# Kernel optimization log

Hardware: AMD Instinct MI355X
Metric: run time of the kernel (lower is better)

## Reference

```python
import jax, jax.numpy as jnp
import numpy as np

B, N, L, D_MODEL, H, D_K, D_V = 8, 307, 64, 64, 4, 16, 16


def setup_inputs() -> dict:
    key = jax.random.key(0)
    ks = jax.random.split(key, 10)
    inp = {
        "input_Q": jax.random.normal(ks[0], (B, N, L, D_MODEL), jnp.float32),
        "input_K": jax.random.normal(ks[1], (B, N, L, D_MODEL), jnp.float32),
        "input_V": jax.random.normal(ks[2], (B, N, L, D_MODEL), jnp.float32),
        "attn_mask": jax.random.uniform(ks[3], (B, N, L, 1), jnp.float32),
        "res_att": jax.random.normal(ks[4], (B, N, H, L, L), jnp.float32),
        # Linear weights stored as [in, out] (torch nn.Linear weight transposed)
        "W_Q": jax.random.normal(ks[5], (D_MODEL, H * D_K), jnp.float32) / np.sqrt(D_MODEL),
        "W_K": jax.random.normal(ks[6], (D_MODEL, H * D_K), jnp.float32) / np.sqrt(D_MODEL),
        "W_V": jax.random.normal(ks[7], (D_MODEL, H * D_V), jnp.float32) / np.sqrt(D_MODEL),
        "W_fc": jax.random.normal(ks[8], (H * D_V, D_MODEL), jnp.float32) / np.sqrt(H * D_V),
        # freshly-constructed nn.LayerNorm has weight=1, bias=0
        "ln_scale": jnp.ones((D_MODEL,), jnp.float32),
        "ln_bias": jnp.zeros((D_MODEL,), jnp.float32),
    }
    return inp


def _layernorm(x, scale, bias, eps=1e-5):
    mu = jnp.mean(x, axis=-1, keepdims=True)
    var = jnp.mean(jnp.square(x - mu), axis=-1, keepdims=True)
    return (x - mu) * jax.lax.rsqrt(var + eps) * scale + bias


def reference(input_Q, input_K, input_V, attn_mask, res_att, W_Q, W_K, W_V, W_fc, ln_scale, ln_bias):
    # projections -> [B,N,H,L,d]
    def proj(x, W, d):
        y = jnp.einsum('bnlf,fe->bnle', x, W)
        return y.reshape(B, N, L, H, d).transpose(0, 1, 3, 2, 4)

    Q = proj(input_Q, W_Q, D_K)
    K = proj(input_K, W_K, D_K)
    V = proj(input_V, W_V, D_V)

    # scaled QK^T + residual attention bias: [B,N,H,Lq,Lk]
    scores = jnp.einsum('bnhqd,bnhkd->bnhqk', Q, K) / np.sqrt(D_K) + res_att
    # attn_mask [B,N,L,1] -> broadcast over heads (axis 2) and key dim (last)
    mask = attn_mask[:, :, None, :, :]  # [B,N,1,L,1]
    scores = jnp.where(mask > 0.5, jnp.float32(-1e9), scores)

    # NOTE: original softmaxes over dim=3 (the query axis), faithful here
    attn = jax.nn.softmax(scores, axis=3)
    context = jnp.einsum('bnhqk,bnhkd->bnhqd', attn, V)
    context = context.transpose(0, 1, 3, 2, 4).reshape(B, N, L, H * D_V)
    output = jnp.einsum('bnlc,cf->bnlf', context, W_fc)
    out = _layernorm(output + input_Q, ln_scale, ln_bias)
    return out, scores
```

## Files before the change

### kernel.cpp

```cpp
#include <hip/hip_runtime.h>

#define B_   8
#define N_   307
#define BN   (B_ * N_)
#define OUT_ELEMS (BN * 64 * 64)

typedef float f32x4 __attribute__((ext_vector_type(4)));
typedef short s16x8 __attribute__((ext_vector_type(8)));

__device__ __forceinline__ unsigned short f2bf(float x) {
    unsigned int u = __builtin_bit_cast(unsigned int, x);
    u += 0x7FFFu + ((u >> 16) & 1u);
    return (unsigned short)(u >> 16);
}

__device__ __forceinline__ void bar_lds() {
    asm volatile("s_waitcnt lgkmcnt(0)\n\ts_barrier" ::: "memory");
}

__device__ __forceinline__ int swz(int row) { return row ^ ((row >> 3) & 7); }

__device__ __forceinline__ s16x8 ldfrag(const unsigned short* p) {
    return *reinterpret_cast<const s16x8*>(p);
}

__device__ __forceinline__ s16x8 cvt8(float4 lo, float4 hi) {
    s16x8 f;
    f[0] = (short)f2bf(lo.x); f[1] = (short)f2bf(lo.y);
    f[2] = (short)f2bf(lo.z); f[3] = (short)f2bf(lo.w);
    f[4] = (short)f2bf(hi.x); f[5] = (short)f2bf(hi.y);
    f[6] = (short)f2bf(hi.z); f[7] = (short)f2bf(hi.w);
    return f;
}

__device__ __forceinline__ void loadW(const float* __restrict__ src,
                                      float4 wvv[4], int tid) {
    const float4* s4 = reinterpret_cast<const float4*>(src);
#pragma unroll
    for (int i = 0; i < 4; ++i) wvv[i] = s4[i * 256 + tid];
}

__device__ __forceinline__ void writeW(const float4 wvv[4],
                                       unsigned short* dst, int tid) {
#pragma unroll
    for (int i = 0; i < 4; ++i) {
        int idx = i * 256 + tid;
        float4 v = wvv[i];
        int k  = idx >> 4;
        int n0 = (idx & 15) << 2;
        int ki = k >> 5;
        int qd = (k >> 3) & 3;
        int j  = k & 7;
        float vv[4] = {v.x, v.y, v.z, v.w};
#pragma unroll
        for (int c = 0; c < 4; ++c) {
            int n = n0 + c;
            int row = ((n >> 4) * 2 + ki) * 64 + (qd << 4) + (n & 15);
            dst[(swz(row) << 3) + j] = f2bf(vv[c]);
        }
    }
}

__global__ __launch_bounds__(256, 4) void mta_kernel(
    const float* __restrict__ Xq, const float* __restrict__ Xk,
    const float* __restrict__ Xv, const float* __restrict__ maskp,
    const float* __restrict__ res, const float* __restrict__ Wq,
    const float* __restrict__ Wk, const float* __restrict__ Wv,
    const float* __restrict__ Wfc, const float* __restrict__ lnS,
    const float* __restrict__ lnB, float* __restrict__ out,
    float* __restrict__ scores_out)
{
    __shared__ __align__(16) unsigned char smem[40960];
    unsigned short* sKf = (unsigned short*)(smem);
    unsigned short* sQf = (unsigned short*)(smem + 8192);
    unsigned short* sVf = (unsigned short*)(smem + 16384);
    unsigned short* sW0 = (unsigned short*)(smem + 24576);
    unsigned short* sW1 = (unsigned short*)(smem + 32768);

    const int bn   = blockIdx.x;
    const int tid  = threadIdx.x;
    const int w    = tid >> 6;
    const int lane = tid & 63;
    const int quad = lane >> 4;
    const int l16  = lane & 15;
    const size_t base64 = (size_t)bn * 4096;

    const int soff0 = l16 * 64 + w * 16 + quad * 4;

    bool bmv[4];
#pragma unroll
    for (int nt = 0; nt < 4; ++nt)
        bmv[nt] = maskp[bn * 64 + nt * 16 + l16] > 0.5f;

    const int xoff = (w * 16 + l16) * 64 + quad * 8;
    float4 wv[4];
    loadW(Wq, wv, tid);
    const float* pX0 = Xq + base64 + xoff;
    float4 x00 = *(const float4*)(pX0),      x01 = *(const float4*)(pX0 + 4);
    float4 x02 = *(const float4*)(pX0 + 32), x03 = *(const float4*)(pX0 + 36);
    f32x4 rA[4];
    {
        const float* rp = res + (((size_t)(bn * 4)) << 12) + soff0;
#pragma unroll
        for (int nt = 0; nt < 4; ++nt)
            rA[nt] = *reinterpret_cast<const f32x4*>(rp + nt * 1024);
    }
    writeW(wv, sW0, tid);
    bar_lds();

    loadW(Wk, wv, tid);
    const float* pX1 = Xk + base64 + xoff;
    float4 x10 = *(const float4*)(pX1),      x11 = *(const float4*)(pX1 + 4);
    float4 x12 = *(const float4*)(pX1 + 32), x13 = *(const float4*)(pX1 + 36);
    {
        s16x8 a0 = cvt8(x00, x01);
        s16x8 a1 = cvt8(x02, x03);
#pragma unroll
        for (int nt = 0; nt < 4; ++nt) {
            f32x4 acc = {0.f, 0.f, 0.f, 0.f};
            s16x8 b0 = ldfrag(sW0 + (swz((nt * 2 + 0) * 64 + lane) << 3));
            s16x8 b1 = ldfrag(sW0 + (swz((nt * 2 + 1) * 64 + lane) << 3));
            acc = __builtin_amdgcn_mfma_f32_16x16x32_bf16(a0, b0, acc, 0, 0, 0);
            acc = __builtin_amdgcn_mfma_f32_16x16x32_bf16(a1, b1, acc, 0, 0, 0);
#pragma unroll
            for (int r = 0; r < 4; ++r) {
                int rowq = (nt * 4 + w) * 32 + ((l16 >> 3) << 4) + quad * 4 + r;
                sQf[(swz(rowq) << 3) + (l16 & 7)] = f2bf(acc[r] * 0.25f);
            }
        }
    }
    writeW(wv, sW1, tid);
    bar_lds();

    loadW(Wv, wv, tid);
    const float* pX2 = Xv + base64 + xoff;
    float4 x20 = *(const float4*)(pX2),      x21 = *(const float4*)(pX2 + 4);
    float4 x22 = *(const float4*)(pX2 + 32), x23 = *(const float4*)(pX2 + 36);
    {
        s16x8 a0 = cvt8(x10, x11);
        s16x8 a1 = cvt8(x12, x13);
#pragma unroll
        for (int nt = 0; nt < 4; ++nt) {
            f32x4 acc = {0.f, 0.f, 0.f, 0.f};
            s16x8 b0 = ldfrag(sW1 + (swz((nt * 2 + 0) * 64 + lane) << 3));
            s16x8 b1 = ldfrag(sW1 + (swz((nt * 2 + 1) * 64 + lane) << 3));
            acc = __builtin_amdgcn_mfma_f32_16x16x32_bf16(a0, b0, acc, 0, 0, 0);
            acc = __builtin_amdgcn_mfma_f32_16x16x32_bf16(a1, b1, acc, 0, 0, 0);
#pragma unroll
            for (int r = 0; r < 4; ++r) {
                int rowk = (nt * 4 + w) * 32 + ((l16 >> 3) << 4) + quad * 4 + r;
                sKf[(swz(rowk) << 3) + (l16 & 7)] = f2bf(acc[r]);
            }
        }
    }
    writeW(wv, sW0, tid);
    bar_lds();

    {
        s16x8 a0 = cvt8(x20, x21);
        s16x8 a1 = cvt8(x22, x23);
#pragma unroll
        for (int nt = 0; nt < 4; ++nt) {
            f32x4 acc = {0.f, 0.f, 0.f, 0.f};
            s16x8 b0 = ldfrag(sW0 + (swz((nt * 2 + 0) * 64 + lane) << 3));
            s16x8 b1 = ldfrag(sW0 + (swz((nt * 2 + 1) * 64 + lane) << 3));
            acc = __builtin_amdgcn_mfma_f32_16x16x32_bf16(a0, b0, acc, 0, 0, 0);
            acc = __builtin_amdgcn_mfma_f32_16x16x32_bf16(a1, b1, acc, 0, 0, 0);
#pragma unroll
            for (int r = 0; r < 4; ++r) {
                int kk = w * 16 + quad * 4 + r;
                int rowv = (nt * 2 + (kk >> 5)) * 64 + (((kk >> 3) & 3) << 4) + l16;
                sVf[(swz(rowv) << 3) + (kk & 7)] = f2bf(acc[r]);
            }
        }
    }
    bar_lds();

    f32x4 ctx[4];
#pragma unroll
    for (int h = 0; h < 4; ++h) ctx[h] = {0.f, 0.f, 0.f, 0.f};

    float4 wfc[4];
    float xres[4][4], scl[4], bia[4];
    const int toff = (w * 16 + quad * 4) * 64 + l16;

    const s16x8 zf = {0, 0, 0, 0, 0, 0, 0, 0};
#pragma unroll
    for (int h = 0; h < 4; ++h) {
        const size_t sbase = ((size_t)(bn * 4 + h)) << 12;
        unsigned short* buf = (h & 1) ? sW1 : sW0;

        s16x8 bk = zf;
        if (lane < 32) bk = ldfrag(sKf + (swz((h * 4 + w) * 32 + lane) << 3));

        f32x4 sr[4];
        float ev[4][4];
        float esum[4] = {0.f, 0.f, 0.f, 0.f};
#pragma unroll
        for (int nt = 0; nt < 4; ++nt) {
            s16x8 aq = zf;
            if (lane < 32) aq = ldfrag(sQf + (swz((h * 4 + nt) * 32 + lane) << 3));
            f32x4 t = __builtin_amdgcn_mfma_f32_16x16x32_bf16(bk, aq, rA[nt], 0, 0, 0);
#pragma unroll
            for (int r = 0; r < 4; ++r) {
                float s = bmv[nt] ? -1e9f : t[r];
                sr[nt][r] = s;
                float e = __expf(s);
                ev[nt][r] = e;
                esum[r] += e;
            }
        }
#pragma unroll
        for (int m = 1; m <= 8; m <<= 1)
#pragma unroll
            for (int r = 0; r < 4; ++r)
                esum[r] += __shfl_xor(esum[r], m, 64);
        float inv[4];
#pragma unroll
        for (int r = 0; r < 4; ++r) inv[r] = 1.0f / (esum[r] + 1e-30f);

#pragma unroll
        for (int nt = 0; nt < 4; ++nt) {
            int row = (nt * 2 + (w >> 1)) * 64 + (((w & 1) << 1) + (quad >> 1)) * 16 + l16;
            short4 pk;
            pk.x = (short)f2bf(ev[nt][0] * inv[0]);
            pk.y = (short)f2bf(ev[nt][1] * inv[1]);
            pk.z = (short)f2bf(ev[nt][2] * inv[2]);
            pk.w = (short)f2bf(ev[nt][3] * inv[3]);
            *reinterpret_cast<short4*>(buf + (swz(row) << 3) + ((quad & 1) << 2)) = pk;
        }
        bar_lds();

        if (h < 3) {
            const float* rp2 = res + sbase + 4096 + soff0;
#pragma unroll
            for (int nt = 0; nt < 4; ++nt)
                rA[nt] = *reinterpret_cast<const f32x4*>(rp2 + nt * 1024);
        } else {
            loadW(Wfc, wfc, tid);
            const float* xp = Xq + base64 + toff;
#pragma unroll
            for (int nt = 0; nt < 4; ++nt) {
#pragma unroll
                for (int r = 0; r < 4; ++r) xres[nt][r] = xp[r * 64 + nt * 16];
                scl[nt] = lnS[nt * 16 + l16];
                bia[nt] = lnB[nt * 16 + l16];
            }
        }
#pragma unroll
        for (int nt = 0; nt < 4; ++nt)
            *reinterpret_cast<f32x4*>(scores_out + sbase + soff0 + nt * 1024) = sr[nt];

#pragma unroll
        for (int ki = 0; ki < 2; ++ki) {
            s16x8 ap = ldfrag(buf + (swz((w * 2 + ki) * 64 + lane) << 3));
            s16x8 bv = ldfrag(sVf + (swz((h * 2 + ki) * 64 + lane) << 3));
            ctx[h] = __builtin_amdgcn_mfma_f32_16x16x32_bf16(ap, bv, ctx[h], 0, 0, 0);
        }
    }
    bar_lds();

#pragma unroll
    for (int hh = 0; hh < 4; ++hh) {
        int c    = hh * 16 + l16;
        int rowb = (w * 2 + (c >> 5)) * 64 + (((c >> 3) & 3) << 4) + quad * 4;
#pragma unroll
        for (int r = 0; r < 4; ++r)
            sKf[(swz(rowb + r) << 3) + (c & 7)] = f2bf(ctx[hh][r]);
    }
    writeW(wfc, sW0, tid);
    bar_lds();

    f32x4 oacc[4];
    {
        s16x8 a0 = ldfrag(sKf + (swz((w * 2 + 0) * 64 + lane) << 3));
        s16x8 a1 = ldfrag(sKf + (swz((w * 2 + 1) * 64 + lane) << 3));
#pragma unroll
        for (int nt = 0; nt < 4; ++nt) {
            f32x4 a = {0.f, 0.f, 0.f, 0.f};
            s16x8 b0 = ldfrag(sW0 + (swz((nt * 2 + 0) * 64 + lane) << 3));
            s16x8 b1 = ldfrag(sW0 + (swz((nt * 2 + 1) * 64 + lane) << 3));
            a = __builtin_amdgcn_mfma_f32_16x16x32_bf16(a0, b0, a, 0, 0, 0);
            a = __builtin_amdgcn_mfma_f32_16x16x32_bf16(a1, b1, a, 0, 0, 0);
            oacc[nt] = a;
        }
    }

#pragma unroll
    for (int r = 0; r < 4; ++r) {
        float px[4], sum = 0.f, sq = 0.f;
#pragma unroll
        for (int nt = 0; nt < 4; ++nt) {
            float x = oacc[nt][r] + xres[nt][r];
            px[nt] = x; sum += x; sq += x * x;
        }
#pragma unroll
        for (int m = 1; m <= 8; m <<= 1) {
            sum += __shfl_xor(sum, m, 64);
            sq  += __shfl_xor(sq,  m, 64);
        }
        float mu   = sum * 0.015625f;
        float var  = sq * 0.015625f - mu * mu;
        float rstd = rsqrtf(var + 1e-5f);
#pragma unroll
        for (int nt = 0; nt < 4; ++nt) {
            out[base64 + toff + r * 64 + nt * 16] = (px[nt] - mu) * rstd * scl[nt] + bia[nt];
        }
    }
}

extern "C" void kernel_launch(void* const* d_in, const int* in_sizes, int n_in,
                              void* d_out, int out_size, void* d_ws, size_t ws_size,
                              hipStream_t stream) {
    const float* Xq   = (const float*)d_in[0];
    const float* Xk   = (const float*)d_in[1];
    const float* Xv   = (const float*)d_in[2];
    const float* msk  = (const float*)d_in[3];
    const float* res  = (const float*)d_in[4];
    const float* Wq   = (const float*)d_in[5];
    const float* Wk   = (const float*)d_in[6];
    const float* Wv   = (const float*)d_in[7];
    const float* Wfc  = (const float*)d_in[8];
    const float* lnS  = (const float*)d_in[9];
    const float* lnB  = (const float*)d_in[10];
    float* out    = (float*)d_out;
    float* scores = out + OUT_ELEMS;
    mta_kernel<<<BN, 256, 0, stream>>>(Xq, Xk, Xv, msk, res, Wq, Wk, Wv, Wfc,
                                       lnS, lnB, out, scores);
}
```

Measured before the change: 103.0 us.

## Process two (b,n) tiles per block to amortize weight staging and barriers

Each block now handles two adjacent (b,n) slices instead of one, so the four weight matrices are loaded and converted to bf16 in LDS once per pair rather than once per slice. Barriers and the per-block setup are also shared across both slices. The softmax now recomputes exp rather than keeping the exponentials in registers. The cost is doubled LDS use (80KB), more live registers, launch bounds lowered to 2 blocks per SM, and half as many blocks, which reduces occupancy and latency hiding on a kernel that is largely memory-bound.

```diff
diff --git a/kernel.cpp b/kernel.cpp
--- a/kernel.cpp
+++ b/kernel.cpp
@@ -3,6 +3,7 @@
 #define B_   8
 #define N_   307
 #define BN   (B_ * N_)
+#define NB2  (BN / 2)
 #define OUT_ELEMS (BN * 64 * 64)
 
 typedef float f32x4 __attribute__((ext_vector_type(4)));
@@ -61,7 +62,93 @@
     }
 }
 
-__global__ __launch_bounds__(256, 4) void mta_kernel(
+template <int PJ>
+__device__ __forceinline__ void proj_tile(const float4 xv[4],
+                                          const unsigned short* wbuf,
+                                          unsigned short* sQf, unsigned short* sKf,
+                                          unsigned short* sVf,
+                                          int w, int lane, int quad, int l16)
+{
+    s16x8 a0 = cvt8(xv[0], xv[1]);
+    s16x8 a1 = cvt8(xv[2], xv[3]);
+#pragma unroll
+    for (int nt = 0; nt < 4; ++nt) {
+        f32x4 acc = {0.f, 0.f, 0.f, 0.f};
+        s16x8 b0 = ldfrag(wbuf + (swz((nt * 2 + 0) * 64 + lane) << 3));
+        s16x8 b1 = ldfrag(wbuf + (swz((nt * 2 + 1) * 64 + lane) << 3));
+        acc = __builtin_amdgcn_mfma_f32_16x16x32_bf16(a0, b0, acc, 0, 0, 0);
+        acc = __builtin_amdgcn_mfma_f32_16x16x32_bf16(a1, b1, acc, 0, 0, 0);
+        if (PJ == 0) {
+#pragma unroll
+            for (int r = 0; r < 4; ++r) {
+                int rowq = (nt * 4 + w) * 32 + ((l16 >> 3) << 4) + quad * 4 + r;
+                sQf[(swz(rowq) << 3) + (l16 & 7)] = f2bf(acc[r] * 0.25f);
+            }
+        } else if (PJ == 1) {
+#pragma unroll
+            for (int r = 0; r < 4; ++r) {
+                int rowk = (nt * 4 + w) * 32 + ((l16 >> 3) << 4) + quad * 4 + r;
+                sKf[(swz(rowk) << 3) + (l16 & 7)] = f2bf(acc[r]);
+            }
+        } else {
+#pragma unroll
+            for (int r = 0; r < 4; ++r) {
+                int kk = w * 16 + quad * 4 + r;
+                int rowv = (nt * 2 + (kk >> 5)) * 64 + (((kk >> 3) & 3) << 4) + l16;
+                sVf[(swz(rowv) << 3) + (kk & 7)] = f2bf(acc[r]);
+            }
+        }
+    }
+}
+
+__device__ __forceinline__ void attn_tile(const unsigned short* sKf,
+                                          const unsigned short* sQf,
+                                          unsigned short* buf,
+                                          const f32x4 rA[4], const bool bmv[4],
+                                          float* __restrict__ sp, int h,
+                                          int w, int lane, int quad, int l16)
+{
+    const s16x8 zf = {0, 0, 0, 0, 0, 0, 0, 0};
+    s16x8 bk = zf;
+    if (lane < 32) bk = ldfrag(sKf + (swz((h * 4 + w) * 32 + lane) << 3));
+    f32x4 sr[4];
+    float esum[4] = {0.f, 0.f, 0.f, 0.f};
+#pragma unroll
+    for (int nt = 0; nt < 4; ++nt) {
+        s16x8 aq = zf;
+        if (lane < 32) aq = ldfrag(sQf + (swz((h * 4 + nt) * 32 + lane) << 3));
+        f32x4 t = __builtin_amdgcn_mfma_f32_16x16x32_bf16(bk, aq, rA[nt], 0, 0, 0);
+#pragma unroll
+        for (int r = 0; r < 4; ++r) {
+            float s = bmv[nt] ? -1e9f : t[r];
+            sr[nt][r] = s;
+            esum[r] += __expf(s);
+        }
+    }
+#pragma unroll
+    for (int m = 1; m <= 8; m <<= 1)
+#pragma unroll
+        for (int r = 0; r < 4; ++r)
+            esum[r] += __shfl_xor(esum[r], m, 64);
+    float inv[4];
+#pragma unroll
+    for (int r = 0; r < 4; ++r) inv[r] = 1.0f / (esum[r] + 1e-30f);
+#pragma unroll
+    for (int nt = 0; nt < 4; ++nt) {
+        int row = (nt * 2 + (w >> 1)) * 64 + (((w & 1) << 1) + (quad >> 1)) * 16 + l16;
+        short4 pk;
+        pk.x = (short)f2bf(__expf(sr[nt][0]) * inv[0]);
+        pk.y = (short)f2bf(__expf(sr[nt][1]) * inv[1]);
+        pk.z = (short)f2bf(__expf(sr[nt][2]) * inv[2]);
+        pk.w = (short)f2bf(__expf(sr[nt][3]) * inv[3]);
+        *reinterpret_cast<short4*>(buf + (swz(row) << 3) + ((quad & 1) << 2)) = pk;
+    }
+#pragma unroll
+    for (int nt = 0; nt < 4; ++nt)
+        *reinterpret_cast<f32x4*>(sp + nt * 1024) = sr[nt];
+}
+
+__global__ __launch_bounds__(256, 2) void mta_kernel(
     const float* __restrict__ Xq, const float* __restrict__ Xk,
     const float* __restrict__ Xv, const float* __restrict__ maskp,
     const float* __restrict__ res, const float* __restrict__ Wq,
@@ -70,241 +157,200 @@
     const float* __restrict__ lnB, float* __restrict__ out,
     float* __restrict__ scores_out)
 {
-    __shared__ __align__(16) unsigned char smem[40960];
-    unsigned short* sKf = (unsigned short*)(smem);
-    unsigned short* sQf = (unsigned short*)(smem + 8192);
-    unsigned short* sVf = (unsigned short*)(smem + 16384);
-    unsigned short* sW0 = (unsigned short*)(smem + 24576);
-    unsigned short* sW1 = (unsigned short*)(smem + 32768);
-
-    const int bn   = blockIdx.x;
+    __shared__ __align__(16) unsigned char smem[81920];
+    unsigned short* sKf0 = (unsigned short*)(smem);
+    unsigned short* sQf0 = (unsigned short*)(smem + 8192);
+    unsigned short* sVf0 = (unsigned short*)(smem + 16384);
+    unsigned short* sKf1 = (unsigned short*)(smem + 24576);
+    unsigned short* sQf1 = (unsigned short*)(smem + 32768);
+    unsigned short* sVf1 = (unsigned short*)(smem + 40960);
+    unsigned short* sWa  = (unsigned short*)(smem + 49152);
+    unsigned short* sWb  = (unsigned short*)(smem + 57344);
+    unsigned short* sWc  = (unsigned short*)(smem + 65536);
+    unsigned short* sWd  = (unsigned short*)(smem + 73728);
+
+    const int bn0  = blockIdx.x * 2;
     const int tid  = threadIdx.x;
     const int w    = tid >> 6;
     const int lane = tid & 63;
     const int quad = lane >> 4;
     const int l16  = lane & 15;
-    const size_t base64 = (size_t)bn * 4096;
+    const size_t base_a = (size_t)bn0 * 4096;
+    const size_t base_b = base_a + 4096;
 
     const int soff0 = l16 * 64 + w * 16 + quad * 4;
-
-    bool bmv[4];
-#pragma unroll
-    for (int nt = 0; nt < 4; ++nt)
-        bmv[nt] = maskp[bn * 64 + nt * 16 + l16] > 0.5f;
-
-    const int xoff = (w * 16 + l16) * 64 + quad * 8;
-    float4 wv[4];
+    const int xoff  = (w * 16 + l16) * 64 + quad * 8;
+
+    bool bma[4], bmb[4];
+#pragma unroll
+    for (int nt = 0; nt < 4; ++nt) {
+        bma[nt] = maskp[bn0 * 64 + nt * 16 + l16] > 0.5f;
+        bmb[nt] = maskp[(bn0 + 1) * 64 + nt * 16 + l16] > 0.5f;
+    }
+
+    f32x4 rAa[4], rAb[4];
+    {
+        const float* ra = res + (((size_t)(bn0 * 4)) << 12) + soff0;
+        const float* rb = res + (((size_t)((bn0 + 1) * 4)) << 12) + soff0;
+#pragma unroll
+        for (int nt = 0; nt < 4; ++nt) {
+            rAa[nt] = *reinterpret_cast<const f32x4*>(ra + nt * 1024);
+            rAb[nt] = *reinterpret_cast<const f32x4*>(rb + nt * 1024);
+        }
+    }
+
+    float4 wv[4], xa[4], xb[4], ya[4], yb[4];
     loadW(Wq, wv, tid);
-    const float* pX0 = Xq + base64 + xoff;
-    float4 x00 = *(const float4*)(pX0),      x01 = *(const float4*)(pX0 + 4);
-    float4 x02 = *(const float4*)(pX0 + 32), x03 = *(const float4*)(pX0 + 36);
-    f32x4 rA[4];
-    {
-        const float* rp = res + (((size_t)(bn * 4)) << 12) + soff0;
-#pragma unroll
-        for (int nt = 0; nt < 4; ++nt)
-            rA[nt] = *reinterpret_cast<const f32x4*>(rp + nt * 1024);
-    }
-    writeW(wv, sW0, tid);
+    {
+        const float* pa = Xq + base_a + xoff;
+        const float* pb = Xq + base_b + xoff;
+        xa[0] = *(const float4*)(pa);      xa[1] = *(const float4*)(pa + 4);
+        xa[2] = *(const float4*)(pa + 32); xa[3] = *(const float4*)(pa + 36);
+        xb[0] = *(const float4*)(pb);      xb[1] = *(const float4*)(pb + 4);
+        xb[2] = *(const float4*)(pb + 32); xb[3] = *(const float4*)(pb + 36);
+    }
+    writeW(wv, sWa, tid);
     bar_lds();
 
     loadW(Wk, wv, tid);
-    const float* pX1 = Xk + base64 + xoff;
-    float4 x10 = *(const float4*)(pX1),      x11 = *(const float4*)(pX1 + 4);
-    float4 x12 = *(const float4*)(pX1 + 32), x13 = *(const float4*)(pX1 + 36);
-    {
-        s16x8 a0 = cvt8(x00, x01);
-        s16x8 a1 = cvt8(x02, x03);
-#pragma unroll
-        for (int nt = 0; nt < 4; ++nt) {
-            f32x4 acc = {0.f, 0.f, 0.f, 0.f};
-            s16x8 b0 = ldfrag(sW0 + (swz((nt * 2 + 0) * 64 + lane) << 3));
-            s16x8 b1 = ldfrag(sW0 + (swz((nt * 2 + 1) * 64 + lane) << 3));
-            acc = __builtin_amdgcn_mfma_f32_16x16x32_bf16(a0, b0, acc, 0, 0, 0);
-            acc = __builtin_amdgcn_mfma_f32_16x16x32_bf16(a1, b1, acc, 0, 0, 0);
-#pragma unroll
-            for (int r = 0; r < 4; ++r) {
-                int rowq = (nt * 4 + w) * 32 + ((l16 >> 3) << 4) + quad * 4 + r;
-                sQf[(swz(rowq) << 3) + (l16 & 7)] = f2bf(acc[r] * 0.25f);
-            }
-        }
-    }
-    writeW(wv, sW1, tid);
+    {
+        const float* pa = Xk + base_a + xoff;
+        const float* pb = Xk + base_b + xoff;
+        ya[0] = *(const float4*)(pa);      ya[1] = *(const float4*)(pa + 4);
+        ya[2] = *(const float4*)(pa + 32); ya[3] = *(const float4*)(pa + 36);
+        yb[0] = *(const float4*)(pb);      yb[1] = *(const float4*)(pb + 4);
+        yb[2] = *(const float4*)(pb + 32); yb[3] = *(const float4*)(pb + 36);
+    }
+    proj_tile<0>(xa, sWa, sQf0, sKf0, sVf0, w, lane, quad, l16);
+    proj_tile<0>(xb, sWa, sQf1, sKf1, sVf1, w, lane, quad, l16);
+    writeW(wv, sWb, tid);
     bar_lds();
 
     loadW(Wv, wv, tid);
-    const float* pX2 = Xv + base64 + xoff;
-    float4 x20 = *(const float4*)(pX2),      x21 = *(const float4*)(pX2 + 4);
-    float4 x22 = *(const float4*)(pX2 + 32), x23 = *(const float4*)(pX2 + 36);
-    {
-        s16x8 a0 = cvt8(x10, x11);
-        s16x8 a1 = cvt8(x12, x13);
-#pragma unroll
-        for (int nt = 0; nt < 4; ++nt) {
-            f32x4 acc = {0.f, 0.f, 0.f, 0.f};
-            s16x8 b0 = ldfrag(sW1 + (swz((nt * 2 + 0) * 64 + lane) << 3));
-            s16x8 b1 = ldfrag(sW1 + (swz((nt * 2 + 1) * 64 + lane) << 3));
-            acc = __builtin_amdgcn_mfma_f32_16x16x32_bf16(a0, b0, acc, 0, 0, 0);
-            acc = __builtin_amdgcn_mfma_f32_16x16x32_bf16(a1, b1, acc, 0, 0, 0);
-#pragma unroll
-            for (int r = 0; r < 4; ++r) {
-                int rowk = (nt * 4 + w) * 32 + ((l16 >> 3) << 4) + quad * 4 + r;
-                sKf[(swz(rowk) << 3) + (l16 & 7)] = f2bf(acc[r]);
-            }
-        }
-    }
-    writeW(wv, sW0, tid);
-    bar_lds();
-
-    {
-        s16x8 a0 = cvt8(x20, x21);
-        s16x8 a1 = cvt8(x22, x23);
-#pragma unroll
-        for (int nt = 0; nt < 4; ++nt) {
-            f32x4 acc = {0.f, 0.f, 0.f, 0.f};
-            s16x8 b0 = ldfrag(sW0 + (swz((nt * 2 + 0) * 64 + lane) << 3));
-            s16x8 b1 = ldfrag(sW0 + (swz((nt * 2 + 1) * 64 + lane) << 3));
-            acc = __builtin_amdgcn_mfma_f32_16x16x32_bf16(a0, b0, acc, 0, 0, 0);
-            acc = __builtin_amdgcn_mfma_f32_16x16x32_bf16(a1, b1, acc, 0, 0, 0);
-#pragma unroll
-            for (int r = 0; r < 4; ++r) {
-                int kk = w * 16 + quad * 4 + r;
-                int rowv = (nt * 2 + (kk >> 5)) * 64 + (((kk >> 3) & 3) << 4) + l16;
-                sVf[(swz(rowv) << 3) + (kk & 7)] = f2bf(acc[r]);
-            }
-        }
-    }
-    bar_lds();
-
-    f32x4 ctx[4];
-#pragma unroll
-    for (int h = 0; h < 4; ++h) ctx[h] = {0.f, 0.f, 0.f, 0.f};
+    {
+        const float* pa = Xv + base_a + xoff;
+        const float* pb = Xv + base_b + xoff;
+        xa[0] = *(const float4*)(pa);      xa[1] = *(const float4*)(pa + 4);
+        xa[2] = *(const float4*)(pa + 32); xa[3] = *(const float4*)(pa + 36);
+        xb[0] = *(const float4*)(pb);      xb[1] = *(const float4*)(pb + 4);
+        xb[2] = *(const float4*)(pb + 32); xb[3] = *(const float4*)(pb + 36);
+    }
+    proj_tile<1>(ya, sWb, sQf0, sKf0, sVf0, w, lane, quad, l16);
+    proj_tile<1>(yb, sWb, sQf1, sKf1, sVf1, w, lane, quad, l16);
+    writeW(wv, sWa, tid);
+    bar_lds();
+
+    proj_tile<2>(xa, sWa, sQf0, sKf0, sVf0, w, lane, quad, l16);
+    proj_tile<2>(xb, sWa, sQf1, sKf1, sVf1, w, lane, quad, l16);
+    bar_lds();
+
+    f32x4 ctxa[4], ctxb[4];
+#pragma unroll
+    for (int h = 0; h < 4; ++h) { ctxa[h] = {0.f,0.f,0.f,0.f}; ctxb[h] = {0.f,0.f,0.f,0.f}; }
 
     float4 wfc[4];
-    float xres[4][4], scl[4], bia[4];
-    const int toff = (w * 16 + quad * 4) * 64 + l16;
-
-    const s16x8 zf = {0, 0, 0, 0, 0, 0, 0, 0};
 #pragma unroll
     for (int h = 0; h < 4; ++h) {
-        const size_t sbase = ((size_t)(bn * 4 + h)) << 12;
-        unsigned short* buf = (h & 1) ? sW1 : sW0;
-
-        s16x8 bk = zf;
-        if (lane < 32) bk = ldfrag(sKf + (swz((h * 4 + w) * 32 + lane) << 3));
-
-        f32x4 sr[4];
-        float ev[4][4];
-        float esum[4] = {0.f, 0.f, 0.f, 0.f};
-#pragma unroll
-        for (int nt = 0; nt < 4; ++nt) {
-            s16x8 aq = zf;
-            if (lane < 32) aq = ldfrag(sQf + (swz((h * 4 + nt) * 32 + lane) << 3));
-            f32x4 t = __builtin_amdgcn_mfma_f32_16x16x32_bf16(bk, aq, rA[nt], 0, 0, 0);
-#pragma unroll
-            for (int r = 0; r < 4; ++r) {
-                float s = bmv[nt] ? -1e9f : t[r];
-                sr[nt][r] = s;
-                float e = __expf(s);
-                ev[nt][r] = e;
-                esum[r] += e;
-            }
-        }
-#pragma unroll
-        for (int m = 1; m <= 8; m <<= 1)
-#pragma unroll
-            for (int r = 0; r < 4; ++r)
-                esum[r] += __shfl_xor(esum[r], m, 64);
-        float inv[4];
-#pragma unroll
-        for (int r = 0; r < 4; ++r) inv[r] = 1.0f / (esum[r] + 1e-30f);
-
-#pragma unroll
-        for (int nt = 0; nt < 4; ++nt) {
-            int row = (nt * 2 + (w >> 1)) * 64 + (((w & 1) << 1) + (quad >> 1)) * 16 + l16;
-            short4 pk;
-            pk.x = (short)f2bf(ev[nt][0] * inv[0]);
-            pk.y = (short)f2bf(ev[nt][1] * inv[1]);
-            pk.z = (short)f2bf(ev[nt][2] * inv[2]);
-            pk.w = (short)f2bf(ev[nt][3] * inv[3]);
-            *reinterpret_cast<short4*>(buf + (swz(row) << 3) + ((quad & 1) << 2)) = pk;
-        }
+        const size_t sba = ((size_t)(bn0 * 4 + h)) << 12;
+        const size_t sbb = sba + 16384;
+        unsigned short* bufA = (h & 1) ? sWc : sWa;
+        unsigned short* bufB = (h & 1) ? sWd : sWb;
+
+        attn_tile(sKf0, sQf0, bufA, rAa, bma, scores_out + sba + soff0, h, w, lane, quad, l16);
+        attn_tile(sKf1, sQf1, bufB, rAb, bmb, scores_out + sbb + soff0, h, w, lane, quad, l16);
         bar_lds();
 
         if (h < 3) {
-            const float* rp2 = res + sbase + 4096 + soff0;
-#pragma unroll
-            for (int nt = 0; nt < 4; ++nt)
-                rA[nt] = *reinterpret_cast<const f32x4*>(rp2 + nt * 1024);
+            const float* ra = res + sba + 4096 + soff0;
+            const float* rb = res + sbb + 4096 + soff0;
+#pragma unroll
+            for (int nt = 0; nt < 4; ++nt) {
+                rAa[nt] = *reinterpret_cast<const f32x4*>(ra + nt * 1024);
+                rAb[nt] = *reinterpret_cast<const f32x4*>(rb + nt * 1024);
+            }
         } else {
             loadW(Wfc, wfc, tid);
-            const float* xp = Xq + base64 + toff;
-#pragma unroll
-            for (int nt = 0; nt < 4; ++nt) {
-#pragma unroll
-                for (int r = 0; r < 4; ++r) xres[nt][r] = xp[r * 64 + nt * 16];
-                scl[nt] = lnS[nt * 16 + l16];
-                bia[nt] = lnB[nt * 16 + l16];
-            }
-        }
-#pragma unroll
-        for (int nt = 0; nt < 4; ++nt)
-            *reinterpret_cast<f32x4*>(scores_out + sbase + soff0 + nt * 1024) = sr[nt];
+        }
 
 #pragma unroll
         for (int ki = 0; ki < 2; ++ki) {
-            s16x8 ap = ldfrag(buf + (swz((w * 2 + ki) * 64 + lane) << 3));
-            s16x8 bv = ldfrag(sVf + (swz((h * 2 + ki) * 64 + lane) << 3));
-            ctx[h] = __builtin_amdgcn_mfma_f32_16x16x32_bf16(ap, bv, ctx[h], 0, 0, 0);
-        }
-    }
-    bar_lds();
-
+            s16x8 apA = ldfrag(bufA + (swz((w * 2 + ki) * 64 + lane) << 3));
+            s16x8 bvA = ldfrag(sVf0 + (swz((h * 2 + ki) * 64 + lane) << 3));
+            ctxa[h] = __builtin_amdgcn_mfma_f32_16x16x32_bf16(apA, bvA, ctxa[h], 0, 0, 0);
+            s16x8 apB = ldfrag(bufB + (swz((w * 2 + ki) * 64 + lane) << 3));
+            s16x8 bvB = ldfrag(sVf1 + (swz((h * 2 + ki) * 64 + lane) << 3));
+            ctxb[h] = __builtin_amdgcn_mfma_f32_16x16x32_bf16(apB, bvB, ctxb[h], 0, 0, 0);
+        }
+    }
+    bar_lds();
+
+    const int toff = (w * 16 + quad * 4) * 64 + l16;
 #pragma unroll
     for (int hh = 0; hh < 4; ++hh) {
         int c    = hh * 16 + l16;
         int rowb = (w * 2 + (c >> 5)) * 64 + (((c >> 3) & 3) << 4) + quad * 4;
 #pragma unroll
-        for (int r = 0; r < 4; ++r)
-            sKf[(swz(rowb + r) << 3) + (c & 7)] = f2bf(ctx[hh][r]);
-    }
-    writeW(wfc, sW0, tid);
-    bar_lds();
-
-    f32x4 oacc[4];
-    {
-        s16x8 a0 = ldfrag(sKf + (swz((w * 2 + 0) * 64 + lane) << 3));
-        s16x8 a1 = ldfrag(sKf + (swz((w * 2 + 1) * 64 + lane) << 3));
+        for (int r = 0; r < 4; ++r) {
+            sKf0[(swz(rowb + r) << 3) + (c & 7)] = f2bf(ctxa[hh][r]);
+            sKf1[(swz(rowb + r) << 3) + (c & 7)] = f2bf(ctxb[hh][r]);
+        }
+    }
+    writeW(wfc, sWa, tid);
+    float xra[4][4], xrb[4][4], scl[4], bia[4];
+    {
+        const float* pa = Xq + base_a + toff;
+        const float* pb = Xq + base_b + toff;
 #pragma unroll
         for (int nt = 0; nt < 4; ++nt) {
-            f32x4 a = {0.f, 0.f, 0.f, 0.f};
-            s16x8 b0 = ldfrag(sW0 + (swz((nt * 2 + 0) * 64 + lane) << 3));
-            s16x8 b1 = ldfrag(sW0 + (swz((nt * 2 + 1) * 64 + lane) << 3));
-            a = __builtin_amdgcn_mfma_f32_16x16x32_bf16(a0, b0, a, 0, 0, 0);
-            a = __builtin_amdgcn_mfma_f32_16x16x32_bf16(a1, b1, a, 0, 0, 0);
-            oacc[nt] = a;
-        }
-    }
-
-#pragma unroll
-    for (int r = 0; r < 4; ++r) {
-        float px[4], sum = 0.f, sq = 0.f;
-#pragma unroll
-        for (int nt = 0; nt < 4; ++nt) {
-            float x = oacc[nt][r] + xres[nt][r];
-            px[nt] = x; sum += x; sq += x * x;
-        }
-#pragma unroll
-        for (int m = 1; m <= 8; m <<= 1) {
-            sum += __shfl_xor(sum, m, 64);
-            sq  += __shfl_xor(sq,  m, 64);
-        }
-        float mu   = sum * 0.015625f;
-        float var  = sq * 0.015625f - mu * mu;
-        float rstd = rsqrtf(var + 1e-5f);
-#pragma unroll
-        for (int nt = 0; nt < 4; ++nt) {
-            out[base64 + toff + r * 64 + nt * 16] = (px[nt] - mu) * rstd * scl[nt] + bia[nt];
+#pragma unroll
+            for (int r = 0; r < 4; ++r) {
+                xra[nt][r] = pa[r * 64 + nt * 16];
+                xrb[nt][r] = pb[r * 64 + nt * 16];
+            }
+            scl[nt] = lnS[nt * 16 + l16];
+            bia[nt] = lnB[nt * 16 + l16];
+        }
+    }
+    bar_lds();
+
+#pragma unroll
+    for (int t = 0; t < 2; ++t) {
+        const unsigned short* sA = (t == 0) ? sKf0 : sKf1;
+        const size_t baseo = (t == 0) ? base_a : base_b;
+        f32x4 oacc[4];
+        {
+            s16x8 a0 = ldfrag(sA + (swz((w * 2 + 0) * 64 + lane) << 3));
+            s16x8 a1 = ldfrag(sA + (swz((w * 2 + 1) * 64 + lane) << 3));
+#pragma unroll
+            for (int nt = 0; nt < 4; ++nt) {
+                f32x4 a = {0.f, 0.f, 0.f, 0.f};
+                s16x8 b0 = ldfrag(sWa + (swz((nt * 2 + 0) * 64 + lane) << 3));
+                s16x8 b1 = ldfrag(sWa + (swz((nt * 2 + 1) * 64 + lane) << 3));
+                a = __builtin_amdgcn_mfma_f32_16x16x32_bf16(a0, b0, a, 0, 0, 0);
+                a = __builtin_amdgcn_mfma_f32_16x16x32_bf16(a1, b1, a, 0, 0, 0);
+                oacc[nt] = a;
+            }
+        }
+#pragma unroll
+        for (int r = 0; r < 4; ++r) {
+            float px[4], sum = 0.f, sq = 0.f;
+#pragma unroll
+            for (int nt = 0; nt < 4; ++nt) {
+                float x = oacc[nt][r] + ((t == 0) ? xra[nt][r] : xrb[nt][r]);
+                px[nt] = x; sum += x; sq += x * x;
+            }
+#pragma unroll
+            for (int m = 1; m <= 8; m <<= 1) {
+                sum += __shfl_xor(sum, m, 64);
+                sq  += __shfl_xor(sq,  m, 64);
+            }
+            float mu   = sum * 0.015625f;
+            float var  = sq * 0.015625f - mu * mu;
+            float rstd = rsqrtf(var + 1e-5f);
+#pragma unroll
+            for (int nt = 0; nt < 4; ++nt) {
+                out[baseo + toff + r * 64 + nt * 16] = (px[nt] - mu) * rstd * scl[nt] + bia[nt];
+            }
         }
     }
 }
@@ -325,6 +371,6 @@
     const float* lnB  = (const float*)d_in[10];
     float* out    = (float*)d_out;
     float* scores = out + OUT_ELEMS;
-    mta_kernel<<<BN, 256, 0, stream>>>(Xq, Xk, Xv, msk, res, Wq, Wk, Wv, Wfc,
-                                       lnS, lnB, out, scores);
-}
+    mta_kernel<<<NB2, 256, 0, stream>>>(Xq, Xk, Xv, msk, res, Wq, Wk, Wv, Wfc,
+                                        lnS, lnB, out, scores);
+}
```

After: 106.6 us. +3.5%, slower.
